# Kernel tuning notes

Measured on AMD Instinct MI355X. Metric: run time of the kernel, lower is better.

Reference implementation:

```python
import jax, jax.numpy as jnp
import numpy as np

B, C_IN, C_OUT, N, MODES, TEMB = 16, 64, 64, 16384, 2048, 512


def setup_inputs() -> dict:
    key = jax.random.key(0)
    k1, k2, k3, k4, k5 = jax.random.split(key, 5)
    scale = 1.0 / (C_IN * C_OUT)
    return {
        "x": jax.random.normal(k1, (B, C_IN, N), dtype=jnp.float32),
        "temb": jax.random.normal(k2, (B, TEMB), dtype=jnp.float32),
        "wr": jax.random.normal(k3, (C_IN, C_OUT, MODES), dtype=jnp.float32) * scale,
        "wi": jax.random.normal(k4, (C_IN, C_OUT, MODES), dtype=jnp.float32) * scale,
        "dense_w": jax.random.normal(k5, (C_IN, TEMB), dtype=jnp.float32) * (1.0 / np.sqrt(TEMB)),
        "dense_b": jnp.zeros((C_IN,), dtype=jnp.float32),
    }


def reference(x, temb, wr, wi, dense_w, dense_b):
    # x: [B, C_in, N] real signal; spectral conv in Fourier space (FNO)
    b, c_in, n = x.shape
    modes = wr.shape[-1]
    x_ft = jnp.fft.rfft(x, axis=-1)  # [B, C_in, N//2+1] complex
    # temb injection: Dense_0(act(temb))[:, :, None], act = SiLU (DDPM-style)
    t = jax.nn.silu(temb) @ dense_w.T + dense_b  # [B, C_in]
    xm = x_ft[..., :modes] + t[:, :, None].astype(x_ft.dtype)
    w = wr + 1j * wi  # [C_in, C_out, modes]
    # contract_dense eq for order-3 input: 'abc,bdc->adc'
    out_m = jnp.einsum("bim,iom->bom", xm, w)  # [B, C_out, modes]
    c_out = w.shape[1]
    out_ft = jnp.zeros((b, c_out, n // 2 + 1), dtype=out_m.dtype)
    out_ft = out_ft.at[..., :modes].set(out_m)
    return jnp.fft.irfft(out_ft, n=n, axis=-1)  # [B, C_out, N]
```

## Files before the change

kernel.cpp:

```cpp
#include <hip/hip_runtime.h>
#include <math.h>

#define NB    16
#define CIN   64
#define COUT  64
#define NN    16384
#define HH    8192
#define MODES 2048
#define TEMBD 512

__device__ __forceinline__ int swz(int e) { return e ^ ((e >> 5) & 31); }
__device__ __forceinline__ int rev13(int x) { return (int)(__brev((unsigned)x) >> 19); }

__device__ __forceinline__ void gl_lds16(const void* gsrc, void* lds) {
  __builtin_amdgcn_global_load_lds(
      (const __attribute__((address_space(1))) void*)gsrc,
      (__attribute__((address_space(3))) void*)lds, 16, 0, 0);
}

__global__ void init_tw_k(float2* __restrict__ tw8, float2* __restrict__ tw16) {
  int j = blockIdx.x * blockDim.x + threadIdx.x;
  if (j < 4096) {
    double a = (2.0 * 3.14159265358979323846 / 8192.0) * (double)j;
    tw8[j] = make_float2((float)cos(a), (float)sin(a));
  }
  if (j < 2048) {
    double a = (2.0 * 3.14159265358979323846 / 16384.0) * (double)j;
    tw16[j] = make_float2((float)cos(a), (float)sin(a));
  }
}

template<int J, int S, int LH_HI>
__device__ __forceinline__ void pass_dif(float* zr, float* zi, int pbase,
                                         const float2* __restrict__ tw) {
  int lh = LH_HI;
#pragma unroll
  for (int half = J / 2; half >= 1; half >>= 1, --lh) {
#pragma unroll
    for (int blk = 0; blk < J; blk += 2 * half) {
#pragma unroll
      for (int q = 0; q < half; ++q) {
        const int j0 = blk + q, j1 = j0 + half;
        const float2 w = tw[(pbase + q * S) << (12 - lh)];
        const float ur = zr[j0], ui = zi[j0];
        const float vr = zr[j1], vi = zi[j1];
        zr[j0] = ur + vr; zi[j0] = ui + vi;
        const float br = ur - vr, bi = ui - vi;
        zr[j1] = br * w.x + bi * w.y;
        zi[j1] = bi * w.x - br * w.y;
      }
    }
  }
}

template<int J, int S, int LH_LO>
__device__ __forceinline__ void pass_dit(float* zr, float* zi, int pbase,
                                         const float2* __restrict__ tw) {
  int lh = LH_LO;
#pragma unroll
  for (int half = 1; half <= J / 2; half <<= 1, ++lh) {
#pragma unroll
    for (int blk = 0; blk < J; blk += 2 * half) {
#pragma unroll
      for (int q = 0; q < half; ++q) {
        const int j0 = blk + q, j1 = j0 + half;
        const float2 w = tw[(pbase + q * S) << (12 - lh)];
        const float vr = zr[j1], vi = zi[j1];
        const float tr = vr * w.x - vi * w.y;
        const float ti = vr * w.y + vi * w.x;
        const float ur = zr[j0], ui = zi[j0];
        zr[j0] = ur + tr; zi[j0] = ui + ti;
        zr[j1] = ur - tr; zi[j1] = ui - ti;
      }
    }
  }
}

__global__ __launch_bounds__(256) void fwd_fft_k(
    const float* __restrict__ x, const float* __restrict__ temb,
    const float* __restrict__ dw, const float* __restrict__ db,
    const float2* __restrict__ tw8, const float2* __restrict__ tw16,
    float2* __restrict__ xm)
{
  __shared__ float re[HH];
  __shared__ float im[HH];
  const int row = blockIdx.x;
  const int b = row >> 6, ci = row & 63;
  const int tid = threadIdx.x;

  float part = 0.f;
  {
    const float* tb = temb + b * TEMBD;
    const float* wrow = dw + ci * TEMBD;
    for (int j = tid; j < TEMBD; j += 256) {
      float v = tb[j];
      part += v * wrow[j] / (1.f + __expf(-v));
    }
    for (int off = 32; off > 0; off >>= 1) part += __shfl_down(part, off, 64);
    if ((tid & 63) == 0) re[tid >> 6] = part;
  }
  __syncthreads();
  const float tval = re[0] + re[1] + re[2] + re[3] + db[ci];
  __syncthreads();

  float zr[32], zi[32];

  const float2* xr = (const float2*)(x + (size_t)row * NN);
#pragma unroll
  for (int g = 0; g < 2; ++g) {
    const int i0 = tid + g * 256;
#pragma unroll
    for (int j = 0; j < 16; ++j) {
      float2 v = xr[i0 + j * 512];
      zr[g * 16 + j] = v.x; zi[g * 16 + j] = v.y;
    }
  }
#pragma unroll
  for (int g = 0; g < 2; ++g) {
    const int i0 = tid + g * 256;
    pass_dif<16, 512, 12>(zr + g * 16, zi + g * 16, i0, tw8);
#pragma unroll
    for (int j = 0; j < 16; ++j) {
      const int e = swz(i0 + j * 512);
      re[e] = zr[g * 16 + j]; im[e] = zi[g * 16 + j];
    }
  }
  __syncthreads();

  {
    const int r = tid & 31;
#pragma unroll
    for (int g = 0; g < 2; ++g) {
      const int base = ((tid >> 5) + g * 8) * 512 + r;
#pragma unroll
      for (int j = 0; j < 16; ++j) {
        const int e = swz(base + j * 32);
        zr[g * 16 + j] = re[e]; zi[g * 16 + j] = im[e];
      }
      pass_dif<16, 32, 8>(zr + g * 16, zi + g * 16, r, tw8);
#pragma unroll
      for (int j = 0; j < 16; ++j) {
        const int e = swz(base + j * 32);
        re[e] = zr[g * 16 + j]; im[e] = zi[g * 16 + j];
      }
    }
  }
  __syncthreads();

  {
    const int base = tid * 32;
#pragma unroll
    for (int j = 0; j < 32; ++j) {
      const int e = swz(base + j);
      zr[j] = re[e]; zi[j] = im[e];
    }
    pass_dif<32, 1, 4>(zr, zi, 0, tw8);
#pragma unroll
    for (int j = 0; j < 32; ++j) {
      const int e = swz(base + j);
      re[e] = zr[j]; im[e] = zi[j];
    }
  }
  __syncthreads();

  float2* xrow = xm + (size_t)row * MODES;
  for (int k = tid; k < MODES; k += 256) {
    const int ka = swz(rev13(k));
    const int kb = swz(rev13((HH - k) & (HH - 1)));
    float Ar = re[ka], Ai = im[ka];
    float Br = re[kb], Bi = -im[kb];
    float Sr = 0.5f * (Ar + Br), Si = 0.5f * (Ai + Bi);
    float Dr = 0.5f * (Ar - Br), Di = 0.5f * (Ai - Bi);
    float2 wv = tw16[k];
    float c = wv.x, s = wv.y;
    float Xr = Sr - s * Dr + c * Di;
    float Xi = Si - s * Di - c * Dr;
    xrow[k] = make_float2(Xr + tval, Xi);
  }
}

__global__ __launch_bounds__(512) void spec_mul_k(
    const float2* __restrict__ xm, const float* __restrict__ wr,
    const float* __restrict__ wi, float2* __restrict__ om)
{
  __shared__ float2 xs[16 * 8 * 32];
  __shared__ float4 wsh[8 * 8 * 16];

  const int tid = threadIdx.x;
  const int mp = tid & 15;
  const int od = (tid >> 4) & 7;
  const int h  = tid >> 7;
  const int wv = tid >> 6;
  const int ln = tid & 63;

  const int m0 = blockIdx.x * 32;
  const int o0 = blockIdx.y * 8;
  const int m2 = m0 + mp * 2;

  float4 acc[4];
#pragma unroll
  for (int j = 0; j < 4; ++j) acc[j] = make_float4(0.f, 0.f, 0.f, 0.f);

  for (int ic = 0; ic < 8; ++ic) {
#pragma unroll
    for (int t = 0; t < 4; ++t) {
      const int r = wv * 16 + t * 4 + (ln >> 4);
      const int b = r >> 3, il = r & 7;
      const float2* src =
          xm + ((size_t)(b * CIN + ic * 8 + il)) * MODES + m0 + (ln & 15) * 2;
      gl_lds16((const void*)src, (void*)((char*)xs + (wv * 16 + t * 4) * 256));
    }
#pragma unroll
    for (int t = 0; t < 2; ++t) {
      const int e = tid + t * 512;
      const int il = e >> 7, eo = (e >> 4) & 7, emp = e & 15;
      const size_t wb =
          ((size_t)((ic * 8 + il) * COUT + o0 + eo)) * MODES + m0 + emp * 2;
      const float2 a = *(const float2*)(wr + wb);
      const float2 c = *(const float2*)(wi + wb);
      wsh[e] = make_float4(a.x, a.y, c.x, c.y);
    }
    __syncthreads();

#pragma unroll
    for (int il = 0; il < 8; ++il) {
      const float4 w4 = wsh[(il * 8 + od) * 16 + mp];
#pragma unroll
      for (int j = 0; j < 4; ++j) {
        const float4 xv = *(const float4*)&xs[((h * 4 + j) * 8 + il) * 32 + mp * 2];
        acc[j].x += xv.x * w4.x - xv.y * w4.z;
        acc[j].y += xv.x * w4.z + xv.y * w4.x;
        acc[j].z += xv.z * w4.y - xv.w * w4.w;
        acc[j].w += xv.z * w4.w + xv.w * w4.y;
      }
    }
    __syncthreads();
  }

  const int o = o0 + od;
#pragma unroll
  for (int j = 0; j < 4; ++j) {
    const int b = h * 4 + j;
    *(float4*)(om + ((size_t)(b * COUT + o)) * MODES + m2) = acc[j];
  }
}

__global__ __launch_bounds__(256) void inv_fft_k(
    const float2* __restrict__ om, const float2* __restrict__ tw8,
    const float2* __restrict__ tw16, float* __restrict__ out)
{
  __shared__ float re[HH];
  __shared__ float im[HH];
  const int row = blockIdx.x;
  const int tid = threadIdx.x;

  for (int q = tid; q < HH; q += 256) { re[q] = 0.f; im[q] = 0.f; }
  __syncthreads();

  const float2* grow = om + (size_t)row * MODES;
  for (int k = tid; k < MODES; k += 256) {
    float2 g = grow[k];
    if (k == 0) {
      float v = 0.5f * g.x;
      re[0] = v; im[0] = v;
    } else {
      float2 wv = tw16[k];
      float Pr = 0.5f * g.x, Pi = 0.5f * g.y;
      float c = wv.x, s = wv.y;
      float sr = -(c * Pi + s * Pr);
      float si =  (c * Pr - s * Pi);
      int ka = swz(rev13(k));
      int kb = swz(rev13(HH - k));
      re[ka] = Pr + sr; im[ka] = Pi + si;
      re[kb] = Pr - sr; im[kb] = -(Pi - si);
    }
  }
  __syncthreads();

  float zr[32], zi[32];

  {
    const int base = tid * 32;
#pragma unroll
    for (int j = 0; j < 32; ++j) {
      const int e = swz(base + j);
      zr[j] = re[e]; zi[j] = im[e];
    }
    pass_dit<32, 1, 0>(zr, zi, 0, tw8);
#pragma unroll
    for (int j = 0; j < 32; ++j) {
      const int e = swz(base + j);
      re[e] = zr[j]; im[e] = zi[j];
    }
  }
  __syncthreads();

  {
    const int r = tid & 31;
#pragma unroll
    for (int g = 0; g < 2; ++g) {
      const int base = ((tid >> 5) + g * 8) * 512 + r;
#pragma unroll
      for (int j = 0; j < 16; ++j) {
        const int e = swz(base + j * 32);
        zr[g * 16 + j] = re[e]; zi[g * 16 + j] = im[e];
      }
      pass_dit<16, 32, 5>(zr + g * 16, zi + g * 16, r, tw8);
#pragma unroll
      for (int j = 0; j < 16; ++j) {
        const int e = swz(base + j * 32);
        re[e] = zr[g * 16 + j]; im[e] = zi[g * 16 + j];
      }
    }
  }
  __syncthreads();

  {
    float2* orow = (float2*)(out + (size_t)row * NN);
    const float sc = 1.0f / 8192.0f;
#pragma unroll
    for (int g = 0; g < 2; ++g) {
      const int i0 = tid + g * 256;
#pragma unroll
      for (int j = 0; j < 16; ++j) {
        const int e = swz(i0 + j * 512);
        zr[g * 16 + j] = re[e]; zi[g * 16 + j] = im[e];
      }
      pass_dit<16, 512, 9>(zr + g * 16, zi + g * 16, i0, tw8);
#pragma unroll
      for (int j = 0; j < 16; ++j) {
        orow[i0 + j * 512] = make_float2(zr[g * 16 + j] * sc, zi[g * 16 + j] * sc);
      }
    }
  }
}

extern "C" void kernel_launch(void* const* d_in, const int* in_sizes, int n_in,
                              void* d_out, int out_size, void* d_ws, size_t ws_size,
                              hipStream_t stream) {
  const float* x    = (const float*)d_in[0];
  const float* temb = (const float*)d_in[1];
  const float* wr   = (const float*)d_in[2];
  const float* wi   = (const float*)d_in[3];
  const float* dw   = (const float*)d_in[4];
  const float* db   = (const float*)d_in[5];
  float* out = (float*)d_out;

  char* ws = (char*)d_ws;
  float2* tw8  = (float2*)ws;
  float2* tw16 = (float2*)(ws + 32768);
  float2* xm   = (float2*)(ws + 65536);
  float2* om   = (float2*)(ws + 65536 + (size_t)16777216);

  hipLaunchKernelGGL(init_tw_k, dim3(16), dim3(256), 0, stream, tw8, tw16);
  hipLaunchKernelGGL(fwd_fft_k, dim3(NB * CIN), dim3(256), 0, stream,
                     x, temb, dw, db, tw8, tw16, xm);
  hipLaunchKernelGGL(spec_mul_k, dim3(MODES / 32, COUT / 8), dim3(512), 0, stream,
                     xm, wr, wi, om);
  hipLaunchKernelGGL(inv_fft_k, dim3(NB * COUT), dim3(256), 0, stream,
                     om, tw8, tw16, out);
}
```

Baseline: 250.3 us.

## Retile spectral multiply to 16-mode blocks and skip unused FFT stores

The spectral-multiply kernel now uses 256-thread blocks covering 16 modes and 8 output channels. Each thread accumulates two adjacent output channels for four batches, and the real and imaginary weights are kept in separate LDS arrays. The change roughly halves the per-block tile, so the grid has twice as many blocks, and it drops the final barrier. In exchange, weight loads become scalar 4-byte reads. The forward FFT also skips writing the final-pass elements whose bit-reversed positions are never read when the first 2048 modes are extracted, which saves LDS stores.

```diff
diff --git a/kernel.cpp b/kernel.cpp
--- a/kernel.cpp
+++ b/kernel.cpp
@@ -157,6 +157,7 @@
     pass_dif<32, 1, 4>(zr, zi, 0, tw8);
 #pragma unroll
     for (int j = 0; j < 32; ++j) {
+      if ((j & 3) == 1 || (j & 3) == 2) continue;
       const int e = swz(base + j);
       re[e] = zr[j]; im[e] = zi[j];
     }
@@ -179,69 +180,73 @@
   }
 }
 
-__global__ __launch_bounds__(512) void spec_mul_k(
+__global__ __launch_bounds__(256) void spec_mul_k(
     const float2* __restrict__ xm, const float* __restrict__ wr,
     const float* __restrict__ wi, float2* __restrict__ om)
 {
-  __shared__ float2 xs[16 * 8 * 32];
-  __shared__ float4 wsh[8 * 8 * 16];
+  __shared__ float2 xs[128 * 16];
+  __shared__ float2 wsr[8 * 16 * 4];
+  __shared__ float2 wsi[8 * 16 * 4];
 
   const int tid = threadIdx.x;
-  const int mp = tid & 15;
-  const int od = (tid >> 4) & 7;
-  const int h  = tid >> 7;
-  const int wv = tid >> 6;
+  const int mm = tid & 15;
+  const int og = (tid >> 4) & 3;
+  const int h  = tid >> 6;
   const int ln = tid & 63;
 
-  const int m0 = blockIdx.x * 32;
+  const int m0 = blockIdx.x * 16;
   const int o0 = blockIdx.y * 8;
-  const int m2 = m0 + mp * 2;
-
-  float4 acc[4];
-#pragma unroll
-  for (int j = 0; j < 4; ++j) acc[j] = make_float4(0.f, 0.f, 0.f, 0.f);
+
+  float2 acc[4][2];
+#pragma unroll
+  for (int j = 0; j < 4; ++j) {
+    acc[j][0] = make_float2(0.f, 0.f);
+    acc[j][1] = make_float2(0.f, 0.f);
+  }
 
   for (int ic = 0; ic < 8; ++ic) {
 #pragma unroll
     for (int t = 0; t < 4; ++t) {
-      const int r = wv * 16 + t * 4 + (ln >> 4);
+      const int r = h * 32 + t * 8 + (ln >> 3);
       const int b = r >> 3, il = r & 7;
       const float2* src =
-          xm + ((size_t)(b * CIN + ic * 8 + il)) * MODES + m0 + (ln & 15) * 2;
-      gl_lds16((const void*)src, (void*)((char*)xs + (wv * 16 + t * 4) * 256));
+          xm + ((size_t)(b * CIN + ic * 8 + il)) * MODES + m0 + (ln & 7) * 2;
+      gl_lds16((const void*)src, (void*)((char*)xs + (h * 32 + t * 8) * 128));
     }
 #pragma unroll
     for (int t = 0; t < 2; ++t) {
-      const int e = tid + t * 512;
-      const int il = e >> 7, eo = (e >> 4) & 7, emp = e & 15;
-      const size_t wb =
-          ((size_t)((ic * 8 + il) * COUT + o0 + eo)) * MODES + m0 + emp * 2;
-      const float2 a = *(const float2*)(wr + wb);
-      const float2 c = *(const float2*)(wi + wb);
-      wsh[e] = make_float4(a.x, a.y, c.x, c.y);
+      const int f = tid + t * 256;
+      const int fm = f & 15, fg = (f >> 4) & 3, fil = f >> 6;
+      const size_t rA =
+          ((size_t)((ic * 8 + fil) * COUT + o0 + fg * 2)) * MODES + m0 + fm;
+      const size_t rB = rA + MODES;
+      wsr[(fil * 16 + fm) * 4 + fg] = make_float2(wr[rA], wr[rB]);
+      wsi[(fil * 16 + fm) * 4 + fg] = make_float2(wi[rA], wi[rB]);
     }
     __syncthreads();
 
 #pragma unroll
     for (int il = 0; il < 8; ++il) {
-      const float4 w4 = wsh[(il * 8 + od) * 16 + mp];
+      const float2 wrp = wsr[(il * 16 + mm) * 4 + og];
+      const float2 wip = wsi[(il * 16 + mm) * 4 + og];
 #pragma unroll
       for (int j = 0; j < 4; ++j) {
-        const float4 xv = *(const float4*)&xs[((h * 4 + j) * 8 + il) * 32 + mp * 2];
-        acc[j].x += xv.x * w4.x - xv.y * w4.z;
-        acc[j].y += xv.x * w4.z + xv.y * w4.x;
-        acc[j].z += xv.z * w4.y - xv.w * w4.w;
-        acc[j].w += xv.z * w4.w + xv.w * w4.y;
-      }
-    }
-    __syncthreads();
-  }
-
-  const int o = o0 + od;
+        const float2 xv = xs[((h * 4 + j) * 8 + il) * 16 + mm];
+        acc[j][0].x += xv.x * wrp.x - xv.y * wip.x;
+        acc[j][0].y += xv.x * wip.x + xv.y * wrp.x;
+        acc[j][1].x += xv.x * wrp.y - xv.y * wip.y;
+        acc[j][1].y += xv.x * wip.y + xv.y * wrp.y;
+      }
+    }
+    if (ic < 7) __syncthreads();
+  }
+
 #pragma unroll
   for (int j = 0; j < 4; ++j) {
     const int b = h * 4 + j;
-    *(float4*)(om + ((size_t)(b * COUT + o)) * MODES + m2) = acc[j];
+    const size_t ob = ((size_t)(b * COUT + o0 + og * 2)) * MODES + m0 + mm;
+    om[ob] = acc[j][0];
+    om[ob + MODES] = acc[j][1];
   }
 }
 
@@ -355,7 +360,7 @@
   hipLaunchKernelGGL(init_tw_k, dim3(16), dim3(256), 0, stream, tw8, tw16);
   hipLaunchKernelGGL(fwd_fft_k, dim3(NB * CIN), dim3(256), 0, stream,
                      x, temb, dw, db, tw8, tw16, xm);
-  hipLaunchKernelGGL(spec_mul_k, dim3(MODES / 32, COUT / 8), dim3(512), 0, stream,
+  hipLaunchKernelGGL(spec_mul_k, dim3(MODES / 16, COUT / 8), dim3(256), 0, stream,
                      xm, wr, wi, om);
   hipLaunchKernelGGL(inv_fft_k, dim3(NB * COUT), dim3(256), 0, stream,
                      om, tw8, tw16, out);
```

Result: no change. 254.5 us (+1.7%).
